# Kernel tuning notes

Measured on AMD Instinct MI355X. Metric: run time of the kernel, lower is better.

The kernel has to match this reference:

```python
import jax, jax.numpy as jnp
import numpy as np

HW = 16          # feature map side before crop
P = HW * HW      # 256 spatial positions
G = 128          # output genetic channels per branch
CROP = 14        # crop size


def feature_genetic(x, idx, oh, ow):
    # x: [B, C, 16, 16]; idx: [G, P] channel index per (group, position);
    # oh, ow: [G] crop offsets in {0,1}
    B = x.shape[0]
    feat = x.reshape(B, x.shape[1], P)                 # [B, C, 256]
    pos = jnp.arange(P)
    picked = feat[:, idx, pos]                         # [B, G, 256]
    grid = picked.reshape(B, G, HW, HW)                # [B, 128, 16, 16]
    ch = jnp.arange(G)
    hidx = oh[:, None] + jnp.arange(CROP)[None, :]     # [G, 14]
    widx = ow[:, None] + jnp.arange(CROP)[None, :]     # [G, 14]
    # fancy-index crop: [B, 128, 14, 14]
    return grid[:, ch[:, None, None], hidx[:, :, None], widx[:, None, :]]


def setup_inputs() -> dict:
    key = jax.random.key(0)
    k1, k3, k5, kw, ki, kh, kw2 = jax.random.split(key, 7)
    B, C = 128, 512
    x1 = jax.random.normal(k1, (B, C, HW, HW), dtype=jnp.float32)
    x3 = jax.random.normal(k3, (B, C, HW, HW), dtype=jnp.float32)
    x5 = jax.random.normal(k5, (B, C, HW, HW), dtype=jnp.float32)
    W = jax.random.normal(kw, (768, 384), dtype=jnp.float32) * 0.02  # 1x1 conv weight
    idx = jax.random.randint(ki, (3, G, P), 0, C, dtype=jnp.int32)
    offh = jax.random.randint(kh, (3, G), 0, 2, dtype=jnp.int32)
    offw = jax.random.randint(kw2, (3, G), 0, 2, dtype=jnp.int32)
    return {"x1": x1, "x3": x3, "x5": x5, "W": W, "idx": idx, "offh": offh, "offw": offw}


def reference(x1, x3, x5, W, idx, offh, offw):
    g1 = feature_genetic(x1, idx[0], offh[0], offw[0])   # [B, 128, 14, 14]
    g3 = feature_genetic(x3, idx[1], offh[1], offw[1])
    g5 = feature_genetic(x5, idx[2], offh[2], offw[2])
    feats = jnp.concatenate((g1, g3, g5), axis=1)        # [B, 384, 14, 14]
    # 1x1 conv (no bias): Conv2d(384, 768, kernel_size=1)
    out = jnp.einsum('bchw,oc->bohw', feats, W)          # [B, 768, 14, 14]
    return out
```

## Files before the change

kernel.cpp:

```cpp
#include <hip/hip_runtime.h>
#include <hip/hip_bf16.h>

#define PIX 256
#define CROP 14
#define HW2 196
#define BB 128
#define CC 512
#define NC 384
#define NO 768
#define CAP 128

typedef __bf16 bf16x8 __attribute__((ext_vector_type(8)));
typedef __bf16 bf16x4 __attribute__((ext_vector_type(4)));
typedef float  f32x4  __attribute__((ext_vector_type(4)));
typedef unsigned int u32;

#define GLOAD_LDS16(src, dst) \
    __builtin_amdgcn_global_load_lds((const __attribute__((address_space(1))) void*)(src), \
                                     (__attribute__((address_space(3))) void*)(dst), 16, 0, 0)

__global__ void wconv_kernel(const float* __restrict__ W, __bf16* __restrict__ Wb) {
    int tid = blockIdx.x * 256 + threadIdx.x;
    Wb[tid] = (__bf16)W[tid];
}

__global__ void fill_kernel(const int* __restrict__ idx, const int* __restrict__ offh,
                            const int* __restrict__ offw, int* __restrict__ cnt,
                            u32* __restrict__ bucket) {
    int tid = blockIdx.x * 256 + threadIdx.x;
    int c3 = tid / HW2;
    int hw = tid - c3 * HW2;
    int i = hw / CROP, j = hw - i * CROP;
    int p = (offh[c3] + i) * 16 + offw[c3] + j;
    int ch = idx[c3 * PIX + p];
    int bkt = (c3 >> 7) * CC + ch;
    int pos = atomicAdd(&cnt[bkt], 1);
    if (pos < CAP) bucket[bkt * CAP + pos] = ((u32)tid << 8) | (u32)p;
}

__global__ __launch_bounds__(256) void scatter_kernel(
        const float* __restrict__ x1, const float* __restrict__ x3,
        const float* __restrict__ x5, const int* __restrict__ cnt,
        const u32* __restrict__ bucket, __bf16* __restrict__ fT) {
    __shared__ float ldsf[64 * 256];
    int bx = blockIdx.x;
    int E = cnt[bx]; if (E > CAP) E = CAP;
    if (E == 0) return;
    int b0 = blockIdx.y * 64;
    int t = bx >> 9, ch = bx & 511;
    const float* x = (t == 0) ? x1 : (t == 1) ? x3 : x5;
    int w = threadIdx.x >> 6, lane = threadIdx.x & 63;

    u32 pk0 = bucket[bx * CAP + lane];
    u32 pk1 = bucket[bx * CAP + 64 + lane];

    for (int i = 0; i < 16; ++i) {
        int r = w * 16 + i;
        const float* src = x + ((size_t)(b0 + r) * CC + ch) * PIX + ((lane ^ (r & 31)) << 2);
        GLOAD_LDS16(src, &ldsf[r * 256]);
    }
    __syncthreads();

    for (int e = w; e < E; e += 4) {
        u32 word = (e < 64) ? __shfl(pk0, e) : __shfl(pk1, e - 64);
        u32 rowhw = word >> 8;
        int p = (int)(word & 255);
        float f = ldsf[lane * 256 + ((((p >> 2) ^ (lane & 31)) << 2) | (p & 3))];
        fT[(size_t)rowhw * BB + b0 + lane] = (__bf16)f;
    }
}

__global__ __launch_bounds__(256) void ftrans_kernel(const __bf16* __restrict__ fT,
                                                     __bf16* __restrict__ feats) {
    __shared__ __bf16 lds[64 * 128];
    int hw = blockIdx.x;
    int c0 = blockIdx.y * 64;
    int t = threadIdx.x;
    int l16 = t & 15;
#pragma unroll
    for (int r4 = 0; r4 < 4; ++r4) {
        int cr = (t >> 4) + r4 * 16;
        bf16x8 v = *(const bf16x8*)(fT + ((size_t)(c0 + cr) * HW2 + hw) * BB + l16 * 8);
        int chunk = l16 ^ ((cr >> 3) & 7);
        *(bf16x8*)&lds[cr * 128 + chunk * 8] = v;
    }
    __syncthreads();
    int cg = t & 7;
#pragma unroll
    for (int r = 0; r < 4; ++r) {
        int b = (t >> 3) + r * 32;
        bf16x8 ov;
#pragma unroll
        for (int k = 0; k < 8; ++k) {
            int c = cg * 8 + k;
            ov[k] = lds[c * 128 + (((b >> 3) ^ cg) * 8) + (b & 7)];
        }
        *(bf16x8*)(feats + ((size_t)b * HW2 + hw) * NC + c0 + cg * 8) = ov;
    }
}

__global__ __launch_bounds__(256) void gemm_kernel(const __bf16* __restrict__ feats,
                                                   const __bf16* __restrict__ Wb,
                                                   float* __restrict__ out) {
    __shared__ __bf16 ldsbuf[16384];
    __bf16* Abuf = ldsbuf;
    __bf16* Bbuf = ldsbuf + 8192;

    const int d = blockIdx.x;
    const int wg = (d & 7) * 147 + (d >> 3);
    const int o_base = (wg % 6) * 128;
    const int m_base = (wg / 6) * 128;

    const int tid = threadIdx.x;
    const int wave = tid >> 6, lane = tid & 63;
    const int wo = wave >> 1, wm = wave & 1;
    const int l15 = lane & 15, g = lane >> 4;
    const int xr = l15 & 7;

    f32x4 acc[4][4] = {};

    for (int kt = 0; kt < 6; ++kt) {
        const int k0g = kt * 64;
#pragma unroll
        for (int it = 0; it < 4; ++it) {
            int ck = tid + it * 256;
            int row = ck >> 3, cc = ck & 7;
            int koff = k0g + ((cc ^ (row & 7)) << 3);
            GLOAD_LDS16(Wb    + (size_t)(o_base + row) * NC + koff, Abuf + ck * 8);
            GLOAD_LDS16(feats + (size_t)(m_base + row) * NC + koff, Bbuf + ck * 8);
        }
        __syncthreads();
#pragma unroll
        for (int k0 = 0; k0 < 64; k0 += 32) {
            const int cb = (k0 >> 3) + g;
            bf16x8 a[4], b[4];
#pragma unroll
            for (int s = 0; s < 4; ++s) {
                int arow = wo * 64 + s * 16 + l15;
                a[s] = *(const bf16x8*)&Abuf[arow * 64 + ((cb ^ xr) << 3)];
                int brow = wm * 64 + s * 16 + l15;
                b[s] = *(const bf16x8*)&Bbuf[brow * 64 + ((cb ^ xr) << 3)];
            }
#pragma unroll
            for (int os = 0; os < 4; ++os)
#pragma unroll
                for (int ms = 0; ms < 4; ++ms)
                    acc[os][ms] = __builtin_amdgcn_mfma_f32_16x16x32_bf16(a[os], b[ms], acc[os][ms], 0, 0, 0);
        }
        __syncthreads();
    }

#pragma unroll
    for (int os = 0; os < 4; ++os)
#pragma unroll
        for (int ms = 0; ms < 4; ++ms) {
            int m = m_base + wm * 64 + ms * 16 + l15;
            int bb = m / HW2;
            int hw = m - bb * HW2;
            int o = o_base + wo * 64 + os * 16 + g * 4;
            float* dst = out + ((size_t)bb * NO + o) * HW2 + hw;
            f32x4 v = acc[os][ms];
            dst[0 * HW2] = v[0];
            dst[1 * HW2] = v[1];
            dst[2 * HW2] = v[2];
            dst[3 * HW2] = v[3];
        }
}

extern "C" void kernel_launch(void* const* d_in, const int* in_sizes, int n_in,
                              void* d_out, int out_size, void* d_ws, size_t ws_size,
                              hipStream_t stream) {
    const float* x1   = (const float*)d_in[0];
    const float* x3   = (const float*)d_in[1];
    const float* x5   = (const float*)d_in[2];
    const float* W    = (const float*)d_in[3];
    const int*   idx  = (const int*)d_in[4];
    const int*   offh = (const int*)d_in[5];
    const int*   offw = (const int*)d_in[6];
    float* out = (float*)d_out;

    char* ws = (char*)d_ws;
    __bf16* fT     = (__bf16*)(ws);
    __bf16* feats  = (__bf16*)(ws + 19267584);
    __bf16* Wb     = (__bf16*)(ws + 38535168);
    int*    cnt    = (int*)   (ws + 39124992);
    u32*    bucket = (u32*)   (ws + 39131136);

    wconv_kernel<<<(NO * NC) / 256, 256, 0, stream>>>(W, Wb);
    hipMemsetAsync(cnt, 0, 1536 * sizeof(int), stream);
    fill_kernel<<<(NC * HW2) / 256, 256, 0, stream>>>(idx, offh, offw, cnt, bucket);
    scatter_kernel<<<dim3(1536, 2), 256, 0, stream>>>(x1, x3, x5, cnt, bucket, fT);
    ftrans_kernel<<<dim3(HW2, 6), 256, 0, stream>>>(fT, feats);
    gemm_kernel<<<1176, 256, 0, stream>>>(feats, Wb, out);
}
```

Measured before the change: 114.4 us.

## Regroup scatter blocks to four channels by sixteen batches

Each scatter block now loads four adjacent source channels for 16 batch rows instead of one channel for 64 batch rows. The grid changes from 1536x2 to 384x8. The extraction loop assigns 16 lanes per bucket entry so each wave handles four entries per step. The aim is to balance work across blocks, since per-channel bucket counts vary, and to raise parallelism per block, at the cost of shorter 32-byte contiguous fT stores per entry.

```diff
diff --git a/kernel.cpp b/kernel.cpp
--- a/kernel.cpp
+++ b/kernel.cpp
@@ -42,31 +42,53 @@
         const float* __restrict__ x1, const float* __restrict__ x3,
         const float* __restrict__ x5, const int* __restrict__ cnt,
         const u32* __restrict__ bucket, __bf16* __restrict__ fT) {
-    __shared__ float ldsf[64 * 256];
+    __shared__ float ldsf[16 * 4 * 256];
     int bx = blockIdx.x;
-    int E = cnt[bx]; if (E > CAP) E = CAP;
-    if (E == 0) return;
-    int b0 = blockIdx.y * 64;
-    int t = bx >> 9, ch = bx & 511;
+    int t = bx >> 7, chq = bx & 127;
+    int b0 = blockIdx.y * 16;
     const float* x = (t == 0) ? x1 : (t == 1) ? x3 : x5;
     int w = threadIdx.x >> 6, lane = threadIdx.x & 63;
-
-    u32 pk0 = bucket[bx * CAP + lane];
-    u32 pk1 = bucket[bx * CAP + 64 + lane];
-
-    for (int i = 0; i < 16; ++i) {
-        int r = w * 16 + i;
-        const float* src = x + ((size_t)(b0 + r) * CC + ch) * PIX + ((lane ^ (r & 31)) << 2);
-        GLOAD_LDS16(src, &ldsf[r * 256]);
+    int bkt0 = t * CC + chq * 4;
+
+    int E0 = cnt[bkt0 + 0]; if (E0 > CAP) E0 = CAP;
+    int E1 = cnt[bkt0 + 1]; if (E1 > CAP) E1 = CAP;
+    int E2 = cnt[bkt0 + 2]; if (E2 > CAP) E2 = CAP;
+    int E3 = cnt[bkt0 + 3]; if (E3 > CAP) E3 = CAP;
+    if ((E0 | E1 | E2 | E3) == 0) return;
+
+    u32 pk0[4], pk1[4];
+#pragma unroll
+    for (int q = 0; q < 4; ++q) {
+        pk0[q] = bucket[(bkt0 + q) * CAP + lane];
+        pk1[q] = bucket[(bkt0 + q) * CAP + 64 + lane];
+    }
+
+#pragma unroll
+    for (int j = 0; j < 16; ++j) {
+        int idx = w * 16 + j;
+        int r = idx >> 2, q = idx & 3;
+        const float* src = x + ((size_t)(b0 + r) * CC + chq * 4 + q) * PIX
+                             + ((lane ^ r) << 2);
+        GLOAD_LDS16(src, &ldsf[(r * 4 + q) * 256]);
     }
     __syncthreads();
 
-    for (int e = w; e < E; e += 4) {
-        u32 word = (e < 64) ? __shfl(pk0, e) : __shfl(pk1, e - 64);
-        u32 rowhw = word >> 8;
-        int p = (int)(word & 255);
-        float f = ldsf[lane * 256 + ((((p >> 2) ^ (lane & 31)) << 2) | (p & 3))];
-        fT[(size_t)rowhw * BB + b0 + lane] = (__bf16)f;
+    int sub = lane >> 4, bl = lane & 15;
+#pragma unroll
+    for (int q = 0; q < 4; ++q) {
+        int Eq = (q == 0) ? E0 : (q == 1) ? E1 : (q == 2) ? E2 : E3;
+        for (int e4 = w * 4; e4 < Eq; e4 += 16) {
+            int e = e4 + sub;
+            u32 w0 = __shfl(pk0[q], e & 63);
+            u32 w1 = __shfl(pk1[q], e & 63);
+            u32 word = (e < 64) ? w0 : w1;
+            if (e < Eq) {
+                u32 rowhw = word >> 8;
+                int p = (int)(word & 255);
+                float f = ldsf[(bl * 4 + q) * 256 + ((((p >> 2) ^ bl) << 2) | (p & 3))];
+                fT[(size_t)rowhw * BB + b0 + bl] = (__bf16)f;
+            }
+        }
     }
 }
 
@@ -189,7 +211,7 @@
     wconv_kernel<<<(NO * NC) / 256, 256, 0, stream>>>(W, Wb);
     hipMemsetAsync(cnt, 0, 1536 * sizeof(int), stream);
     fill_kernel<<<(NC * HW2) / 256, 256, 0, stream>>>(idx, offh, offw, cnt, bucket);
-    scatter_kernel<<<dim3(1536, 2), 256, 0, stream>>>(x1, x3, x5, cnt, bucket, fT);
+    scatter_kernel<<<dim3(384, 8), 256, 0, stream>>>(x1, x3, x5, cnt, bucket, fT);
     ftrans_kernel<<<dim3(HW2, 6), 256, 0, stream>>>(fT, feats);
     gemm_kernel<<<1176, 256, 0, stream>>>(feats, Wb, out);
 }
```

Result: no change. 116.1 us (+1.5%).
